# Kernel optimization log

Measured on AMD Instinct MI355X. Metric: run time of the kernel, lower is better.

## Reference

```python
import jax, jax.numpy as jnp
import numpy as np

T, E, H, V, K = 1024, 300, 512, 100000, 12
START, STOP = 10, 11


def setup_inputs() -> dict:
    key = jax.random.key(0)
    ks = jax.random.split(key, 12)
    s = 0.05
    sentence = jax.random.randint(ks[0], (T,), 0, V, dtype=jnp.int32)
    tags = jax.random.randint(ks[1], (T,), 0, START, dtype=jnp.int32)  # real tags only
    word_embeds = jax.random.normal(ks[2], (V, E), jnp.float32) * 0.1

    def lstm_p(k):
        k1, k2 = jax.random.split(k)
        return (jax.random.normal(k1, (4 * H, E), jnp.float32) * s,
                jax.random.normal(k2, (4 * H, H), jnp.float32) * s,
                jnp.zeros(4 * H, jnp.float32), jnp.zeros(4 * H, jnp.float32))

    Wih_f, Whh_f, bih_f, bhh_f = lstm_p(ks[3])
    Wih_b, Whh_b, bih_b, bhh_b = lstm_p(ks[4])
    D = 2 * H
    attn_W = jax.random.normal(ks[5], (D, D), jnp.float32) * s
    attn_b = jnp.zeros(D, jnp.float32)
    h2h1_W = jax.random.normal(ks[6], (D, 2 * D), jnp.float32) * s
    h2h1_b = jnp.zeros(D, jnp.float32)
    tag_W = jax.random.normal(ks[7], (K, D), jnp.float32) * s
    tag_b = jnp.zeros(K, jnp.float32)
    transitions = jax.random.normal(ks[8], (K, K), jnp.float32) * 0.01
    transitions = transitions.at[START, :].set(-10000.0).at[:, STOP].set(-10000.0)
    return dict(sentence=sentence, tags=tags, word_embeds=word_embeds,
                Wih_f=Wih_f, Whh_f=Whh_f, bih_f=bih_f, bhh_f=bhh_f,
                Wih_b=Wih_b, Whh_b=Whh_b, bih_b=bih_b, bhh_b=bhh_b,
                attn_W=attn_W, attn_b=attn_b, h2h1_W=h2h1_W, h2h1_b=h2h1_b,
                tag_W=tag_W, tag_b=tag_b, transitions=transitions)


def _lstm_pass(x, Wih, Whh, bih, bhh):
    # x: [T, E] -> hs: [T, H]   (PyTorch LSTM gate order i,f,g,o)
    xg = x @ Wih.T + bih  # [T, 4H] precomputed input contribution

    def step(carry, g_in):
        h, c = carry
        g = g_in + h @ Whh.T + bhh
        i, f, gg, o = jnp.split(g, 4)
        i = jax.nn.sigmoid(i); f = jax.nn.sigmoid(f)
        gg = jnp.tanh(gg); o = jax.nn.sigmoid(o)
        c = f * c + i * gg
        h = o * jnp.tanh(c)
        return (h, c), h

    init = (jnp.zeros(H, x.dtype), jnp.zeros(H, x.dtype))
    _, hs = jax.lax.scan(step, init, xg)
    return hs


def reference(sentence, tags, word_embeds, Wih_f, Whh_f, bih_f, bhh_f,
              Wih_b, Whh_b, bih_b, bhh_b, attn_W, attn_b,
              h2h1_W, h2h1_b, tag_W, tag_b, transitions):
    x = word_embeds[sentence]                       # [T, E]  (dropout is eval no-op)
    h_fwd = _lstm_pass(x, Wih_f, Whh_f, bih_f, bhh_f)
    h_bwd = _lstm_pass(x[::-1], Wih_b, Whh_b, bih_b, bhh_b)[::-1]
    enc = jnp.concatenate([h_fwd, h_bwd], axis=-1)  # [T, 2H]

    # Attn 'general': energy(t, i) = enc[t] . (W enc[i] + b); vectorized per-timestep loop
    proj = enc @ attn_W.T + attn_b                  # [T, 2H]
    scores = enc @ proj.T                           # [T, T]
    w = jax.nn.softmax(scores, axis=-1)
    ctx = w @ enc                                   # [T, 2H]

    h1 = jnp.tanh(jnp.concatenate([enc, ctx], axis=-1) @ h2h1_W.T + h2h1_b)  # [T, 2H]
    feats = h1 @ tag_W.T + tag_b                    # [T, K]

    # CRF forward algorithm (log partition); transitions[to, from]
    alpha0 = jnp.full((K,), -10000.0, feats.dtype).at[START].set(0.0)

    def crf_step(alpha, feat):
        a = jax.nn.logsumexp(alpha[None, :] + transitions, axis=1) + feat
        return a, None

    alpha, _ = jax.lax.scan(crf_step, alpha0, feats)
    logZ = jax.nn.logsumexp(alpha + transitions[STOP])

    # gold path score (_score_sentence)
    pad_start = jnp.concatenate([jnp.array([START], tags.dtype), tags])
    pad_stop = jnp.concatenate([tags, jnp.array([STOP], tags.dtype)])
    gold = transitions[pad_stop, pad_start].sum() + feats[jnp.arange(T), tags].sum()

    return logZ - gold  # CRF negative log-likelihood for this sentence
```

## Files before the change

kernel.cpp:

```cpp
#include <hip/hip_runtime.h>
#include <hip/hip_fp16.h>

#define T_LEN 1024
#define E_DIM 300
#define H_DIM 512
#define D_DIM 1024
#define K_TAGS 12
#define G4 2048

typedef __attribute__((ext_vector_type(8))) short short8x;
typedef __attribute__((ext_vector_type(4))) float f32x4;

static __device__ __forceinline__ float frcp(float x){ return __builtin_amdgcn_rcpf(x); }
static __device__ __forceinline__ float sigm(float x){ return frcp(1.f + __expf(-x)); }
static __device__ __forceinline__ float ftanh(float x){
  const float e = __expf(2.f * fabsf(x));
  const float t = 1.f - 2.f * frcp(e + 1.f);
  return copysignf(t, x);
}
static __device__ __forceinline__ unsigned short f2b(float f){
  unsigned u = __float_as_uint(f);
  return (unsigned short)((u + 0x7fffu + ((u >> 16) & 1u)) >> 16);
}
static __device__ __forceinline__ uint4 pack8(const float* s){
  uint4 o;
  o.x = (unsigned)f2b(s[0]) | ((unsigned)f2b(s[1]) << 16);
  o.y = (unsigned)f2b(s[2]) | ((unsigned)f2b(s[3]) << 16);
  o.z = (unsigned)f2b(s[4]) | ((unsigned)f2b(s[5]) << 16);
  o.w = (unsigned)f2b(s[6]) | ((unsigned)f2b(s[7]) << 16);
  return o;
}

__global__ void k_gather(const int* __restrict__ sent, const float* __restrict__ we,
                         float* __restrict__ x){
  int idx = blockIdx.x*256 + threadIdx.x;
  if (idx < T_LEN*E_DIM){
    int t = idx / E_DIM, e = idx - t*E_DIM;
    x[idx] = we[(size_t)sent[t]*E_DIM + e];
  }
}

__global__ void k_init(unsigned* __restrict__ hbuf){
  int i = blockIdx.x*256 + threadIdx.x;
  if (i < 2048) hbuf[i] = 0u;
}

__global__ __launch_bounds__(256) void k_gemm_mfma(
    const float* __restrict__ Af, int lda, int arev,
    const float* __restrict__ Bf, const unsigned short* __restrict__ Bh, int ldb,
    const float* __restrict__ bias, int act,
    float* __restrict__ C, int ldc, int M, int N, int K)
{
  __shared__ __align__(16) unsigned short As[64*40];
  __shared__ __align__(16) unsigned short Bs[64*40];
  const int tid = threadIdx.x;
  const int bm = blockIdx.y*64, bn = blockIdx.x*64;
  const int r  = tid >> 2, c8 = (tid & 3) * 8;
  const int wave = tid >> 6, lane = tid & 63;
  const int wm = (wave >> 1) * 32, wn = (wave & 1) * 32;
  const int col = lane & 15, quad = lane >> 4;

  const int am = arev ? (M-1-(bm+r)) : (bm+r);
  const float* arow = Af + (size_t)am*lda;
  const float* brow = Bf ? (Bf + (size_t)(bn+r)*ldb) : (const float*)0;
  const unsigned short* brh = Bh ? (Bh + (size_t)(bn+r)*ldb) : (const unsigned short*)0;

  uint4* aw = (uint4*)(As + r*40 + c8);
  uint4* bw = (uint4*)(Bs + r*40 + c8);

  f32x4 acc[2][2];
  #pragma unroll
  for (int i=0;i<2;i++)
    #pragma unroll
    for (int j=0;j<2;j++) acc[i][j] = (f32x4){0.f,0.f,0.f,0.f};

  for (int k0 = 0; k0 < K; k0 += 32){
    uint4 avv, bvv;
    if (k0 + 32 <= K){
      avv = pack8(arow + k0 + c8);
      bvv = Bh ? *(const uint4*)(brh + k0 + c8) : pack8(brow + k0 + c8);
    } else {
      float ta[8], tb[8];
      #pragma unroll
      for (int i=0;i<8;i++){
        const int kk = k0 + c8 + i;
        ta[i] = (kk < K) ? arow[kk] : 0.f;
        tb[i] = (kk < K && Bf) ? brow[kk] : 0.f;
      }
      avv = pack8(ta); bvv = pack8(tb);
    }
    if (k0) __syncthreads();
    *aw = avv; *bw = bvv;
    __syncthreads();
    const short8x a0 = *(const short8x*)(As + (wm+col)*40    + quad*8);
    const short8x a1 = *(const short8x*)(As + (wm+16+col)*40 + quad*8);
    const short8x b0 = *(const short8x*)(Bs + (wn+col)*40    + quad*8);
    const short8x b1 = *(const short8x*)(Bs + (wn+16+col)*40 + quad*8);
    acc[0][0] = __builtin_amdgcn_mfma_f32_16x16x32_bf16(a0, b0, acc[0][0], 0, 0, 0);
    acc[0][1] = __builtin_amdgcn_mfma_f32_16x16x32_bf16(a0, b1, acc[0][1], 0, 0, 0);
    acc[1][0] = __builtin_amdgcn_mfma_f32_16x16x32_bf16(a1, b0, acc[1][0], 0, 0, 0);
    acc[1][1] = __builtin_amdgcn_mfma_f32_16x16x32_bf16(a1, b1, acc[1][1], 0, 0, 0);
  }

  #pragma unroll
  for (int mt=0;mt<2;mt++){
    #pragma unroll
    for (int nt=0;nt<2;nt++){
      const int cc = bn + wn + 16*nt + col;
      const float bs = bias ? bias[cc] : 0.f;
      #pragma unroll
      for (int i=0;i<4;i++){
        const int rr = bm + wm + 16*mt + quad*4 + i;
        float v = acc[mt][nt][i] + bs;
        if (act) v = ftanh(v);
        C[(size_t)rr*ldc + cc] = v;
      }
    }
  }
}

__global__ __launch_bounds__(256, 1) void k_lstm(
    const float* __restrict__ Whh_f, const float* __restrict__ Whh_b,
    const float* __restrict__ bih_f, const float* __restrict__ bhh_f,
    const float* __restrict__ bih_b, const float* __restrict__ bhh_b,
    const float* __restrict__ xg_f, const float* __restrict__ xg_b,
    unsigned* __restrict__ hbuf, float* __restrict__ enc)
{
  const int dir = blockIdx.x >> 5;
  const int w   = blockIdx.x & 31;
  const int tid = threadIdx.x;
  const int wave = tid >> 6, lane = tid & 63;
  const int col = lane & 15, quad = lane >> 4;

  const float* Whh = dir ? Whh_b : Whh_f;
  const float* xg  = dir ? xg_b  : xg_f;

  const int rowA = wave*H_DIM + w*16 + col;
  short8x w_frag[16];
  #pragma unroll
  for (int s=0;s<16;s++){
    const float* bp = Whh + (size_t)rowA*H_DIM + s*32 + quad*8;
    uint4 u = pack8(bp);
    w_frag[s] = *reinterpret_cast<short8x*>(&u);
  }

  float bias_r = 0.f, xg_cur = 0.f, c_reg = 0.f;
  int row2 = 0;
  if (tid < 64){
    row2 = (tid >> 4)*H_DIM + w*16 + (tid & 15);
    bias_r = dir ? (bih_b[row2] + bhh_b[row2]) : (bih_f[row2] + bhh_f[row2]);
    xg_cur = xg[row2];
  }

  __shared__ __align__(16) unsigned short lds_hb[512];
  __shared__ __align__(16) float raw[64];

  unsigned* hb = hbuf + dir*1024;

  for (int t = 1; t <= T_LEN; ++t){
    {
      unsigned* s0 = hb + ((t-1)&1)*512 + tid;
      const unsigned want = (unsigned)(t-1);
      unsigned v0 = __hip_atomic_load(s0,     __ATOMIC_RELAXED, __HIP_MEMORY_SCOPE_AGENT);
      unsigned v1 = __hip_atomic_load(s0+256, __ATOMIC_RELAXED, __HIP_MEMORY_SCOPE_AGENT);
      while (((v0 >> 16) != want) || ((v1 >> 16) != want)){
        v0 = __hip_atomic_load(s0,     __ATOMIC_RELAXED, __HIP_MEMORY_SCOPE_AGENT);
        v1 = __hip_atomic_load(s0+256, __ATOMIC_RELAXED, __HIP_MEMORY_SCOPE_AGENT);
      }
      lds_hb[tid]     = f2b(__half2float(__ushort_as_half((unsigned short)(v0 & 0xffffu))));
      lds_hb[tid+256] = f2b(__half2float(__ushort_as_half((unsigned short)(v1 & 0xffffu))));
    }
    __syncthreads();

    float xg_nxt = 0.f;
    if (tid < 64 && t < T_LEN) xg_nxt = xg[(size_t)t*G4 + row2];

    f32x4 a0 = (f32x4){0.f,0.f,0.f,0.f}, a1 = (f32x4){0.f,0.f,0.f,0.f};
    #pragma unroll
    for (int s=0;s<16;s+=2){
      const short8x b0 = *(const short8x*)(lds_hb + s*32     + quad*8);
      const short8x b1 = *(const short8x*)(lds_hb + (s+1)*32 + quad*8);
      a0 = __builtin_amdgcn_mfma_f32_16x16x32_bf16(w_frag[s],   b0, a0, 0, 0, 0);
      a1 = __builtin_amdgcn_mfma_f32_16x16x32_bf16(w_frag[s+1], b1, a1, 0, 0, 0);
    }
    if (col == 0){
      f32x4 asum = a0 + a1;
      *reinterpret_cast<f32x4*>(raw + wave*16 + quad*4) = asum;
    }
    __syncthreads();

    if (tid < 64){
      float v = raw[tid] + bias_r + xg_cur;
      const float va = ((tid >> 4) == 2) ? ftanh(v) : sigm(v);
      const int l2 = tid & 15;
      const float iv = __shfl(va, l2);
      const float fv = __shfl(va, l2 + 16);
      const float gg = __shfl(va, l2 + 32);
      const float ov = __shfl(va, l2 + 48);
      if (tid < 16){
        c_reg = fv*c_reg + iv*gg;
        const float hh = ov*ftanh(c_reg);
        const int hj = w*16 + tid;
        const unsigned hv = ((unsigned)t << 16) |
                            (unsigned)__half_as_ushort(__float2half(hh));
        __hip_atomic_store(hb + (t&1)*512 + hj, hv,
                           __ATOMIC_RELAXED, __HIP_MEMORY_SCOPE_AGENT);
        const int tt = dir ? (T_LEN - t) : (t - 1);
        enc[(size_t)tt*D_DIM + dir*H_DIM + hj] = hh;
      }
      xg_cur = xg_nxt;
    }
    __syncthreads();
  }
}

__global__ __launch_bounds__(256) void k_softmax(float* __restrict__ S){
  float* r = S + (size_t)blockIdx.x*1024;
  const int tid = threadIdx.x;
  float v[4];
  #pragma unroll
  for (int i=0;i<4;i++) v[i] = r[tid + i*256];
  float m = fmaxf(fmaxf(v[0],v[1]), fmaxf(v[2],v[3]));
  #pragma unroll
  for (int off=32; off>=1; off>>=1) m = fmaxf(m, __shfl_xor(m, off));
  __shared__ float red[4], red2[4];
  const int wid = tid >> 6, lane = tid & 63;
  if (lane == 0) red[wid] = m;
  __syncthreads();
  m = fmaxf(fmaxf(red[0],red[1]), fmaxf(red[2],red[3]));
  float s = 0.f;
  #pragma unroll
  for (int i=0;i<4;i++){ v[i] = __expf(v[i]-m); s += v[i]; }
  #pragma unroll
  for (int off=32; off>=1; off>>=1) s += __shfl_xor(s, off);
  if (lane == 0) red2[wid] = s;
  __syncthreads();
  s = red2[0]+red2[1]+red2[2]+red2[3];
  const float inv = frcp(s);
  #pragma unroll
  for (int i=0;i<4;i++) r[tid + i*256] = v[i]*inv;
}

__global__ void k_copy_enc(const float* __restrict__ enc, float* __restrict__ cat){
  int idx = blockIdx.x*256 + threadIdx.x;
  if (idx < T_LEN*D_DIM){
    int t = idx >> 10, d = idx & 1023;
    cat[(size_t)t*2048 + d] = enc[idx];
  }
}

__global__ __launch_bounds__(256) void k_castT(const float* __restrict__ src,
                                               unsigned short* __restrict__ dst){
  __shared__ float tile[32][33];
  const int bx = blockIdx.x*32, by = blockIdx.y*32;
  const int tx = threadIdx.x & 31, ty8 = threadIdx.x >> 5;
  #pragma unroll
  for (int i=ty8;i<32;i+=8) tile[i][tx] = src[(size_t)(by+i)*1024 + bx+tx];
  __syncthreads();
  #pragma unroll
  for (int i=ty8;i<32;i+=8) dst[(size_t)(bx+i)*1024 + by+tx] = f2b(tile[tx][i]);
}

__global__ __launch_bounds__(256) void k_feats(
    const float* __restrict__ h1, const float* __restrict__ tagW,
    const float* __restrict__ tagb, float* __restrict__ feats)
{
  const int t = blockIdx.x;
  const int wave = threadIdx.x >> 6, lane = threadIdx.x & 63;
  const float* hr = h1 + (size_t)t*D_DIM;
  float hv[16];
  #pragma unroll
  for (int i=0;i<16;i++) hv[i] = hr[lane + 64*i];
  #pragma unroll
  for (int j=0;j<3;j++){
    const int tag = wave*3 + j;
    const float* wr = tagW + (size_t)tag*D_DIM;
    float s = 0.f;
    #pragma unroll
    for (int i=0;i<16;i++) s += hv[i]*wr[lane + 64*i];
    #pragma unroll
    for (int off=32; off>=1; off>>=1) s += __shfl_xor(s, off);
    if (lane == 0) feats[(size_t)t*K_TAGS + tag] = s + tagb[tag];
  }
}

__global__ void k_crf(const float* __restrict__ feats, const float* __restrict__ trans,
                      const int* __restrict__ tags, float* __restrict__ out){
  const int tid = threadIdx.x;
  float gold = 0.f;
  for (int i = tid; i <= T_LEN; i += 64){
    const int to = (i < T_LEN) ? tags[i]   : 11;
    const int fr = (i == 0)    ? 10        : tags[i-1];
    gold += trans[to*K_TAGS + fr];
    if (i < T_LEN) gold += feats[(size_t)i*K_TAGS + tags[i]];
  }
  #pragma unroll
  for (int off=32; off>=1; off>>=1) gold += __shfl_xor(gold, off);

  float Trow[K_TAGS];
  if (tid < K_TAGS){
    #pragma unroll
    for (int j=0;j<K_TAGS;j++) Trow[j] = trans[tid*K_TAGS + j];
  }
  float alpha = (tid == 10) ? 0.f : -10000.f;
  for (int t=0;t<T_LEN;++t){
    float av[K_TAGS];
    #pragma unroll
    for (int j=0;j<K_TAGS;j++) av[j] = __shfl(alpha, j);
    if (tid < K_TAGS){
      float vv[K_TAGS], m = -1e30f;
      #pragma unroll
      for (int j=0;j<K_TAGS;j++){ vv[j] = av[j] + Trow[j]; m = fmaxf(m, vv[j]); }
      float s = 0.f;
      #pragma unroll
      for (int j=0;j<K_TAGS;j++) s += __expf(vv[j]-m);
      alpha = m + __logf(s) + feats[(size_t)t*K_TAGS + tid];
    }
  }
  float v = (tid < K_TAGS) ? (alpha + trans[11*K_TAGS + tid]) : -1e30f;
  float m = v;
  #pragma unroll
  for (int off=32; off>=1; off>>=1) m = fmaxf(m, __shfl_xor(m, off));
  float e = (tid < K_TAGS) ? __expf(v - m) : 0.f;
  #pragma unroll
  for (int off=32; off>=1; off>>=1) e += __shfl_xor(e, off);
  if (tid == 0) out[0] = (m + __logf(e)) - gold;
}

extern "C" void kernel_launch(void* const* d_in, const int* in_sizes, int n_in,
                              void* d_out, int out_size, void* d_ws, size_t ws_size,
                              hipStream_t stream)
{
  const int*   sentence = (const int*)d_in[0];
  const int*   tags     = (const int*)d_in[1];
  const float* we       = (const float*)d_in[2];
  const float* Wih_f    = (const float*)d_in[3];
  const float* Whh_f    = (const float*)d_in[4];
  const float* bih_f    = (const float*)d_in[5];
  const float* bhh_f    = (const float*)d_in[6];
  const float* Wih_b    = (const float*)d_in[7];
  const float* Whh_b    = (const float*)d_in[8];
  const float* bih_b    = (const float*)d_in[9];
  const float* bhh_b    = (const float*)d_in[10];
  const float* attn_W   = (const float*)d_in[11];
  const float* attn_b   = (const float*)d_in[12];
  const float* h2h1_W   = (const float*)d_in[13];
  const float* h2h1_b   = (const float*)d_in[14];
  const float* tag_W    = (const float*)d_in[15];
  const float* tag_b    = (const float*)d_in[16];
  const float* trans    = (const float*)d_in[17];
  float* out = (float*)d_out;

  float* ws     = (float*)d_ws;
  float* cat    = ws;
  float* reg2   = cat  + 2097152;
  float* enc    = reg2 + 2097152;
  float* proj   = enc  + 1048576;
  float* feats  = proj + 1048576;
  unsigned* hbuf= (unsigned*)(feats + 12288);
  float* xg_f   = cat;
  float* xg_b   = reg2;
  float* scores = reg2;
  float* h1     = reg2 + 1048576;
  float* x      = proj;
  unsigned short* encT = (unsigned short*)proj;

  k_gather<<<dim3((T_LEN*E_DIM + 255)/256), dim3(256), 0, stream>>>(sentence, we, x);
  k_init<<<dim3(8), dim3(256), 0, stream>>>(hbuf);
  k_gemm_mfma<<<dim3(32,16), dim3(256), 0, stream>>>(x, E_DIM, 0,
      Wih_f, nullptr, E_DIM, nullptr, 0, xg_f, G4, T_LEN, G4, E_DIM);
  k_gemm_mfma<<<dim3(32,16), dim3(256), 0, stream>>>(x, E_DIM, 1,
      Wih_b, nullptr, E_DIM, nullptr, 0, xg_b, G4, T_LEN, G4, E_DIM);
  k_lstm<<<dim3(64), dim3(256), 0, stream>>>(Whh_f, Whh_b, bih_f, bhh_f,
      bih_b, bhh_b, xg_f, xg_b, hbuf, enc);
  k_gemm_mfma<<<dim3(16,16), dim3(256), 0, stream>>>(enc, D_DIM, 0,
      attn_W, nullptr, D_DIM, attn_b, 0, proj, D_DIM, T_LEN, D_DIM, D_DIM);
  k_gemm_mfma<<<dim3(16,16), dim3(256), 0, stream>>>(enc, D_DIM, 0,
      proj, nullptr, D_DIM, nullptr, 0, scores, T_LEN, T_LEN, T_LEN, D_DIM);
  k_softmax<<<dim3(1024), dim3(256), 0, stream>>>(scores);
  k_copy_enc<<<dim3(4096), dim3(256), 0, stream>>>(enc, cat);
  k_castT<<<dim3(32,32), dim3(256), 0, stream>>>(enc, encT);
  k_gemm_mfma<<<dim3(16,16), dim3(256), 0, stream>>>(scores, T_LEN, 0,
      nullptr, encT, D_DIM, nullptr, 0, cat + 1024, 2048, T_LEN, D_DIM, T_LEN);
  k_gemm_mfma<<<dim3(16,16), dim3(256), 0, stream>>>(cat, 2048, 0,
      h2h1_W, nullptr, 2048, h2h1_b, 1, h1, D_DIM, T_LEN, D_DIM, 2048);
  k_feats<<<dim3(1024), dim3(256), 0, stream>>>(h1, tag_W, tag_b, feats);
  k_crf<<<dim3(1), dim3(64), 0, stream>>>(feats, trans, tags, out);
}
```

Before: 2.158 ms.

## Parallelize CRF scan via chunked log-semiring matrices; exchange LSTM h as bf16

The serial 1024-step CRF forward recursion is split into 64 chunks. Each block composes 16 steps into a 12x12 log-semiring transfer matrix, and a second kernel scans the 64 matrices while a separate wave computes the gold path score. This cuts the sequential dependency chain in the CRF by about 16x, at the cost of an extra launch and more total arithmetic. The LSTM also now publishes h as bf16 instead of fp16, which removes the per-step half-to-bf16 conversion on the critical recurrent path but lowers the precision of the exchanged hidden state.

After: 1.859 ms. 1.16x faster.

```diff
diff --git a/kernel.cpp b/kernel.cpp
--- a/kernel.cpp
+++ b/kernel.cpp
@@ -167,8 +167,8 @@
         v0 = __hip_atomic_load(s0,     __ATOMIC_RELAXED, __HIP_MEMORY_SCOPE_AGENT);
         v1 = __hip_atomic_load(s0+256, __ATOMIC_RELAXED, __HIP_MEMORY_SCOPE_AGENT);
       }
-      lds_hb[tid]     = f2b(__half2float(__ushort_as_half((unsigned short)(v0 & 0xffffu))));
-      lds_hb[tid+256] = f2b(__half2float(__ushort_as_half((unsigned short)(v1 & 0xffffu))));
+      lds_hb[tid]     = (unsigned short)(v0 & 0xffffu);
+      lds_hb[tid+256] = (unsigned short)(v1 & 0xffffu);
     }
     __syncthreads();
 
@@ -201,8 +201,7 @@
         c_reg = fv*c_reg + iv*gg;
         const float hh = ov*ftanh(c_reg);
         const int hj = w*16 + tid;
-        const unsigned hv = ((unsigned)t << 16) |
-                            (unsigned)__half_as_ushort(__float2half(hh));
+        const unsigned hv = ((unsigned)t << 16) | (unsigned)f2b(hh);
         __hip_atomic_store(hb + (t&1)*512 + hj, hv,
                            __ATOMIC_RELAXED, __HIP_MEMORY_SCOPE_AGENT);
         const int tt = dir ? (T_LEN - t) : (t - 1);
@@ -284,47 +283,97 @@
   }
 }
 
-__global__ void k_crf(const float* __restrict__ feats, const float* __restrict__ trans,
-                      const int* __restrict__ tags, float* __restrict__ out){
-  const int tid = threadIdx.x;
-  float gold = 0.f;
-  for (int i = tid; i <= T_LEN; i += 64){
-    const int to = (i < T_LEN) ? tags[i]   : 11;
-    const int fr = (i == 0)    ? 10        : tags[i-1];
-    gold += trans[to*K_TAGS + fr];
-    if (i < T_LEN) gold += feats[(size_t)i*K_TAGS + tags[i]];
-  }
-  #pragma unroll
-  for (int off=32; off>=1; off>>=1) gold += __shfl_xor(gold, off);
-
-  float Trow[K_TAGS];
-  if (tid < K_TAGS){
-    #pragma unroll
-    for (int j=0;j<K_TAGS;j++) Trow[j] = trans[tid*K_TAGS + j];
-  }
-  float alpha = (tid == 10) ? 0.f : -10000.f;
-  for (int t=0;t<T_LEN;++t){
-    float av[K_TAGS];
-    #pragma unroll
-    for (int j=0;j<K_TAGS;j++) av[j] = __shfl(alpha, j);
-    if (tid < K_TAGS){
-      float vv[K_TAGS], m = -1e30f;
-      #pragma unroll
-      for (int j=0;j<K_TAGS;j++){ vv[j] = av[j] + Trow[j]; m = fmaxf(m, vv[j]); }
-      float s = 0.f;
-      #pragma unroll
-      for (int j=0;j<K_TAGS;j++) s += __expf(vv[j]-m);
-      alpha = m + __logf(s) + feats[(size_t)t*K_TAGS + tid];
-    }
-  }
-  float v = (tid < K_TAGS) ? (alpha + trans[11*K_TAGS + tid]) : -1e30f;
-  float m = v;
-  #pragma unroll
-  for (int off=32; off>=1; off>>=1) m = fmaxf(m, __shfl_xor(m, off));
-  float e = (tid < K_TAGS) ? __expf(v - m) : 0.f;
-  #pragma unroll
-  for (int off=32; off>=1; off>>=1) e += __shfl_xor(e, off);
-  if (tid == 0) out[0] = (m + __logf(e)) - gold;
+__global__ __launch_bounds__(64) void k_crf1(const float* __restrict__ feats,
+                                             const float* __restrict__ trans,
+                                             float* __restrict__ chunkM){
+  const int c = blockIdx.x;
+  const int r = threadIdx.x;
+  __shared__ float sT[144];
+  __shared__ float sF[16*12];
+  for (int i=r; i<144; i+=64) sT[i] = trans[i];
+  const int t0 = c*16;
+  for (int i=r; i<192; i+=64) sF[i] = feats[(size_t)t0*K_TAGS + i];
+  __syncthreads();
+  if (r < 12){
+    float m[12], nm[12];
+    #pragma unroll
+    for (int k=0;k<12;k++) m[k] = sT[k*12 + r] + sF[k];
+    for (int s=1; s<16; ++s){
+      #pragma unroll
+      for (int i=0;i<12;i++){
+        float v[12]; float mx = -1e30f;
+        #pragma unroll
+        for (int k=0;k<12;k++){ v[k] = sT[i*12+k] + m[k]; mx = fmaxf(mx, v[k]); }
+        float ss = 0.f;
+        #pragma unroll
+        for (int k=0;k<12;k++) ss += __expf(v[k]-mx);
+        nm[i] = sF[s*12+i] + mx + __logf(ss);
+      }
+      #pragma unroll
+      for (int i=0;i<12;i++) m[i] = nm[i];
+    }
+    #pragma unroll
+    for (int k=0;k<12;k++) chunkM[c*144 + k*12 + r] = m[k];
+  }
+}
+
+__global__ __launch_bounds__(128) void k_crf2(const float* __restrict__ chunkM,
+                                              const float* __restrict__ feats,
+                                              const float* __restrict__ trans,
+                                              const int* __restrict__ tags,
+                                              float* __restrict__ out){
+  const int tid = threadIdx.x, wave = tid >> 6, lane = tid & 63;
+  __shared__ float sGold;
+  float alpha = (lane == 10) ? 0.f : -10000.f;
+  if (wave == 1){
+    float g = 0.f;
+    for (int i = lane; i <= T_LEN; i += 64){
+      const int to = (i < T_LEN) ? tags[i]   : 11;
+      const int fr = (i == 0)    ? 10        : tags[i-1];
+      g += trans[to*K_TAGS + fr];
+      if (i < T_LEN) g += feats[(size_t)i*K_TAGS + tags[i]];
+    }
+    #pragma unroll
+    for (int off=32; off>=1; off>>=1) g += __shfl_xor(g, off);
+    if (lane == 0) sGold = g;
+  } else {
+    float pf[12];
+    #pragma unroll
+    for (int k=0;k<12;k++) pf[k] = (lane < 12) ? chunkM[lane*12 + k] : 0.f;
+    for (int c=0; c<64; ++c){
+      float av[12];
+      #pragma unroll
+      for (int j=0;j<12;j++) av[j] = __shfl(alpha, j);
+      float cur[12];
+      #pragma unroll
+      for (int k=0;k<12;k++) cur[k] = pf[k];
+      if (c+1 < 64){
+        #pragma unroll
+        for (int k=0;k<12;k++)
+          pf[k] = (lane < 12) ? chunkM[(c+1)*144 + lane*12 + k] : 0.f;
+      }
+      if (lane < 12){
+        float v[12]; float mx = -1e30f;
+        #pragma unroll
+        for (int k=0;k<12;k++){ v[k] = cur[k] + av[k]; mx = fmaxf(mx, v[k]); }
+        float ss = 0.f;
+        #pragma unroll
+        for (int k=0;k<12;k++) ss += __expf(v[k]-mx);
+        alpha = mx + __logf(ss);
+      }
+    }
+  }
+  __syncthreads();
+  if (wave == 0){
+    float v = (lane < K_TAGS) ? (alpha + trans[11*K_TAGS + lane]) : -1e30f;
+    float m = v;
+    #pragma unroll
+    for (int off=32; off>=1; off>>=1) m = fmaxf(m, __shfl_xor(m, off));
+    float e = (lane < K_TAGS) ? __expf(v - m) : 0.f;
+    #pragma unroll
+    for (int off=32; off>=1; off>>=1) e += __shfl_xor(e, off);
+    if (lane == 0) out[0] = (m + __logf(e)) - sGold;
+  }
 }
 
 extern "C" void kernel_launch(void* const* d_in, const int* in_sizes, int n_in,
@@ -364,6 +413,7 @@
   float* h1     = reg2 + 1048576;
   float* x      = proj;
   unsigned short* encT = (unsigned short*)proj;
+  float* chunkM = proj + 524288;
 
   k_gather<<<dim3((T_LEN*E_DIM + 255)/256), dim3(256), 0, stream>>>(sentence, we, x);
   k_init<<<dim3(8), dim3(256), 0, stream>>>(hbuf);
@@ -385,5 +435,6 @@
   k_gemm_mfma<<<dim3(16,16), dim3(256), 0, stream>>>(cat, 2048, 0,
       h2h1_W, nullptr, 2048, h2h1_b, 1, h1, D_DIM, T_LEN, D_DIM, 2048);
   k_feats<<<dim3(1024), dim3(256), 0, stream>>>(h1, tag_W, tag_b, feats);
-  k_crf<<<dim3(1), dim3(64), 0, stream>>>(feats, trans, tags, out);
-}
+  k_crf1<<<dim3(64), dim3(64), 0, stream>>>(feats, trans, chunkM);
+  k_crf2<<<dim3(1), dim3(128), 0, stream>>>(chunkM, feats, trans, tags, out);
+}
```
